# Performance work log

Measured on AMD Instinct MI355X. Metric: run time of the kernel, lower is better.

Reference implementation:

```python
import jax, jax.numpy as jnp
import numpy as np

# Static conv / spline hyperparameters (match init_kwargs)
KH = KW = 3
SH = SW = 1          # stride
DH = DW = 1          # dilation
GRID_SIZE = 5
SPLINE_ORDER = 3
N_CONVS = 8


def _extract_patches(x):
    """im2col unfold. x: (B,C,H,W) -> (B,C,Ho,Wo,KH*KW), valid padding."""
    B, C, H, W = x.shape
    Ho = (H - (KH - 1) * DH - 1) // SH + 1
    Wo = (W - (KW - 1) * DW - 1) // SW + 1
    cols = []
    for i in range(KH):
        for j in range(KW):
            cols.append(x[:, :,
                          i * DH: i * DH + (Ho - 1) * SH + 1: SH,
                          j * DW: j * DW + (Wo - 1) * SW + 1: SW])
    return jnp.stack(cols, axis=-1), Ho, Wo


def _b_splines(xf, grid):
    """Cox-de Boor recursion. xf: (P,K), grid: (K, G+2*so+1) -> (P,K,G+so)."""
    x = xf[:, :, None]
    bases = ((x >= grid[:, :-1]) & (x < grid[:, 1:])).astype(xf.dtype)
    for k in range(1, SPLINE_ORDER + 1):
        bases = ((x - grid[:, :-(k + 1)]) / (grid[:, k:-1] - grid[:, :-(k + 1)])
                 * bases[:, :, :-1]
                 + (grid[:, k + 1:] - x) / (grid[:, k + 1:] - grid[:, 1:-k])
                 * bases[:, :, 1:])
    return bases


def setup_inputs() -> dict:
    key = jax.random.key(0)
    k0, k1, k2, k3 = jax.random.split(key, 4)
    B, C, H, W = 8, 32, 64, 64
    K = KH * KW                       # in_features of KANLinear = 9
    coeff = GRID_SIZE + SPLINE_ORDER  # spline coefficients per input = 8
    # activations inside grid_range [-1, 1]
    x = jax.random.uniform(k0, (B, C, H, W), jnp.float32, -1.0, 1.0)
    # grid buffer: arange(-so, gs+so+1)*h + grid_range[0], tiled per input feature
    h = (1.0 - (-1.0)) / GRID_SIZE
    g = jnp.arange(-SPLINE_ORDER, GRID_SIZE + SPLINE_ORDER + 1,
                   dtype=jnp.float32) * h - 1.0
    grid = jnp.tile(g[None, :], (K, 1))  # (K, 12)
    base_weight = jax.random.normal(k1, (N_CONVS, K), jnp.float32) / np.sqrt(K)
    spline_weight = jax.random.normal(k2, (N_CONVS, K, coeff), jnp.float32) * 0.1
    spline_scaler = jax.random.normal(k3, (N_CONVS, K), jnp.float32) / np.sqrt(K) + 1.0
    return {"x": x, "grid": grid, "base_weight": base_weight,
            "spline_weight": spline_weight, "spline_scaler": spline_scaler}


def reference(x, grid, base_weight, spline_weight, spline_scaler):
    B, C, H, W = x.shape
    patches, Ho, Wo = _extract_patches(x)          # (B,C,Ho,Wo,K)
    K = KH * KW
    xf = patches.reshape(-1, K)                    # (P, K), P = B*C*Ho*Wo
    # KANLinear: base path (SiLU + linear) + spline path (B-spline basis + linear)
    base_out = jnp.einsum('pk,vk->pv', jax.nn.silu(xf), base_weight)
    bases = _b_splines(xf, grid)                   # (P, K, coeff)
    scaled_sw = spline_weight * spline_scaler[:, :, None]
    spline_out = jnp.einsum('pkc,vkc->pv', bases, scaled_sw)
    out = (base_out + spline_out).reshape(B, C, Ho, Wo, N_CONVS)
    # channel-major then conv ordering: out[:, kern + channel*n_convs]
    return out.transpose(0, 1, 4, 2, 3).reshape(B, C * N_CONVS, Ho, Wo)
```

## Files before the change

### kernel.cpp

```cpp
#include <hip/hip_runtime.h>

typedef _Float16 f16;
typedef _Float16 f16x8 __attribute__((ext_vector_type(8)));
typedef float    f32x4 __attribute__((ext_vector_type(4)));

#define HO 62
#define WO 62

__global__ __launch_bounds__(512, 4) void kan_conv_mfma(
    const float* __restrict__ x,
    const float* __restrict__ grid,
    const float* __restrict__ bw,
    const float* __restrict__ sw,
    const float* __restrict__ sc,
    float* __restrict__ out)
{
    __shared__ __align__(16) f16 feat[19456];

    const int tid  = threadIdx.x;
    const int lane = tid & 63;
    const int w    = tid >> 6;

    const int bx    = blockIdx.x;
    const int plane = bx >> 2;
    const int chunk = bx & 3;
    const int r0    = (chunk < 3) ? chunk * 16 : 46;

    const int nn = lane & 15;
    const int kb = lane >> 4;
    f16x8 bfrag[3][2];
    #pragma unroll
    for (int ki = 0; ki < 3; ++ki) {
        #pragma unroll
        for (int kjp = 0; kjp < 2; ++kjp) {
            f16x8 bf;
            #pragma unroll
            for (int e = 0; e < 8; ++e) {
                const int k    = kb * 8 + e;
                const int kj   = kjp * 2 + (k >> 4);
                const int slot = k & 15;
                float wv = 0.0f;
                if (nn < 8 && kj < 3 && slot < 9) {
                    const int kk = ki * 3 + kj;
                    wv = (slot == 0) ? bw[nn * 9 + kk]
                                     : sw[(nn * 9 + kk) * 8 + (slot - 1)] * sc[nn * 9 + kk];
                }
                bf[e] = (f16)wv;
            }
            bfrag[ki][kjp] = bf;
        }
    }

    const float g0    = grid[0];
    const float inv_h = 1.0f / (grid[1] - grid[0]);
    const float* xp   = x + (size_t)plane * 4096;

    for (int idx = tid; idx < 18 * 64; idx += 512) {
        const int row = idx >> 6;
        const int col = idx & 63;
        const float xv = xp[(r0 + row) * 64 + col];

        const float s = xv / (1.0f + __expf(-xv));
        const float u = (xv - g0) * inv_h;
        int j = (int)floorf(u);
        j = (j < 3) ? 3 : ((j > 7) ? 7 : j);
        const float t   = u - (float)j;
        const float omt = 1.0f - t;
        const float t2  = t * t;
        const float t3  = t2 * t;
        const float c6  = 1.0f / 6.0f;
        float bv[4];
        bv[0] = omt * omt * omt * c6;
        bv[1] = (3.0f * t3 - 6.0f * t2 + 4.0f) * c6;
        bv[2] = (-3.0f * t3 + 3.0f * t2 + 3.0f * t + 1.0f) * c6;
        bv[3] = t3 * c6;

        const int base0 = row * 1024 + col * 8;
        f16x8 z0 = {(f16)s, (f16)0.f, (f16)0.f, (f16)0.f,
                    (f16)0.f, (f16)0.f, (f16)0.f, (f16)0.f};
        f16x8 z1 = {(f16)0.f, (f16)0.f, (f16)0.f, (f16)0.f,
                    (f16)0.f, (f16)0.f, (f16)0.f, (f16)0.f};
        *(f16x8*)&feat[base0]       = z0;
        *(f16x8*)&feat[base0 + 512] = z1;
        #pragma unroll
        for (int m = 0; m < 4; ++m) {
            const int slot = j - 2 + m;
            feat[row * 1024 + (slot >> 3) * 512 + col * 8 + (slot & 7)] = (f16)bv[m];
        }
    }
    for (int idx = tid; idx < 128; idx += 512) {
        f16x8 z = {(f16)0.f, (f16)0.f, (f16)0.f, (f16)0.f,
                   (f16)0.f, (f16)0.f, (f16)0.f, (f16)0.f};
        *(f16x8*)&feat[18432 + idx * 8] = z;
    }
    __syncthreads();

    const int mI    = lane & 15;
    const int khalf = kb & 1;
    const int cAdd  = kb >> 1;

    for (int u = w; u < 64; u += 8) {
        const int ro = u >> 2;
        const int c0 = (u & 3) * 16;
        f32x4 acc = {0.f, 0.f, 0.f, 0.f};
        #pragma unroll
        for (int ki = 0; ki < 3; ++ki) {
            #pragma unroll
            for (int kjp = 0; kjp < 2; ++kjp) {
                const int col = c0 + mI + kjp * 2 + cAdd;
                const f16x8 a = *(const f16x8*)&feat[(ro + ki) * 1024 + khalf * 512 + col * 8];
                acc = __builtin_amdgcn_mfma_f32_16x16x32_f16(a, bfrag[ki][kjp], acc, 0, 0, 0);
            }
        }
        if (nn < 8) {
            const int rowg = r0 + ro;
            const int colb = c0 + kb * 4;
            float* po = out + ((size_t)(plane * 8 + nn) * (HO * WO)) + rowg * WO + colb;
            if (c0 < 48) {
                float2 lo = {acc[0], acc[1]};
                float2 hi = {acc[2], acc[3]};
                *(float2*)po       = lo;
                *(float2*)(po + 2) = hi;
            } else {
                #pragma unroll
                for (int i = 0; i < 4; ++i)
                    if (colb + i < WO) po[i] = acc[i];
            }
        }
    }
}

extern "C" void kernel_launch(void* const* d_in, const int* in_sizes, int n_in,
                              void* d_out, int out_size, void* d_ws, size_t ws_size,
                              hipStream_t stream) {
    const float* x    = (const float*)d_in[0];
    const float* grid = (const float*)d_in[1];
    const float* bw   = (const float*)d_in[2];
    const float* sw   = (const float*)d_in[3];
    const float* sc   = (const float*)d_in[4];
    float* out = (float*)d_out;

    kan_conv_mfma<<<1024, 512, 0, stream>>>(x, grid, bw, sw, sc, out);
}
```

Measured before the change: 94.18 us.

## Split planes into 8-row tiles and reuse A fragments across rows in registers

```diff
diff --git a/kernel.cpp b/kernel.cpp
--- a/kernel.cpp
+++ b/kernel.cpp
@@ -7,7 +7,7 @@
 #define HO 62
 #define WO 62
 
-__global__ __launch_bounds__(512, 4) void kan_conv_mfma(
+__global__ __launch_bounds__(256, 4) void kan_conv_mfma2(
     const float* __restrict__ x,
     const float* __restrict__ grid,
     const float* __restrict__ bw,
@@ -15,16 +15,16 @@
     const float* __restrict__ sc,
     float* __restrict__ out)
 {
-    __shared__ __align__(16) f16 feat[19456];
+    __shared__ __align__(16) f16 feat[10368];
 
     const int tid  = threadIdx.x;
     const int lane = tid & 63;
     const int w    = tid >> 6;
 
     const int bx    = blockIdx.x;
-    const int plane = bx >> 2;
-    const int chunk = bx & 3;
-    const int r0    = (chunk < 3) ? chunk * 16 : 46;
+    const int plane = bx >> 3;
+    const int chunk = bx & 7;
+    const int r0    = chunk * 8;
 
     const int nn = lane & 15;
     const int kb = lane >> 4;
@@ -55,10 +55,11 @@
     const float inv_h = 1.0f / (grid[1] - grid[0]);
     const float* xp   = x + (size_t)plane * 4096;
 
-    for (int idx = tid; idx < 18 * 64; idx += 512) {
+    for (int idx = tid; idx < 640; idx += 256) {
         const int row = idx >> 6;
         const int col = idx & 63;
-        const float xv = xp[(r0 + row) * 64 + col];
+        int gy = r0 + row; gy = (gy < 64) ? gy : 63;
+        const float xv = xp[gy * 64 + col];
 
         const float s = xv / (1.0f + __expf(-xv));
         const float u = (xv - g0) * inv_h;
@@ -88,43 +89,54 @@
             feat[row * 1024 + (slot >> 3) * 512 + col * 8 + (slot & 7)] = (f16)bv[m];
         }
     }
-    for (int idx = tid; idx < 128; idx += 512) {
+    if (tid < 16) {
         f16x8 z = {(f16)0.f, (f16)0.f, (f16)0.f, (f16)0.f,
                    (f16)0.f, (f16)0.f, (f16)0.f, (f16)0.f};
-        *(f16x8*)&feat[18432 + idx * 8] = z;
+        *(f16x8*)&feat[10240 + tid * 8] = z;
     }
     __syncthreads();
 
     const int mI    = lane & 15;
     const int khalf = kb & 1;
     const int cAdd  = kb >> 1;
+    const int c0    = w * 16;
+    const int aBase = khalf * 512 + (c0 + mI + cAdd) * 8;
 
-    for (int u = w; u < 64; u += 8) {
-        const int ro = u >> 2;
-        const int c0 = (u & 3) * 16;
+    f16x8 af[3][2];
+    #pragma unroll
+    for (int kjp = 0; kjp < 2; ++kjp) {
+        af[0][kjp] = *(const f16x8*)&feat[aBase + kjp * 16 + 0 * 1024];
+        af[1][kjp] = *(const f16x8*)&feat[aBase + kjp * 16 + 1 * 1024];
+    }
+
+    #pragma unroll
+    for (int i = 0; i < 8; ++i) {
+        #pragma unroll
+        for (int kjp = 0; kjp < 2; ++kjp)
+            af[(i + 2) % 3][kjp] = *(const f16x8*)&feat[aBase + kjp * 16 + (i + 2) * 1024];
+
         f32x4 acc = {0.f, 0.f, 0.f, 0.f};
         #pragma unroll
         for (int ki = 0; ki < 3; ++ki) {
             #pragma unroll
-            for (int kjp = 0; kjp < 2; ++kjp) {
-                const int col = c0 + mI + kjp * 2 + cAdd;
-                const f16x8 a = *(const f16x8*)&feat[(ro + ki) * 1024 + khalf * 512 + col * 8];
-                acc = __builtin_amdgcn_mfma_f32_16x16x32_f16(a, bfrag[ki][kjp], acc, 0, 0, 0);
-            }
+            for (int kjp = 0; kjp < 2; ++kjp)
+                acc = __builtin_amdgcn_mfma_f32_16x16x32_f16(
+                          af[(i + ki) % 3][kjp], bfrag[ki][kjp], acc, 0, 0, 0);
         }
-        if (nn < 8) {
-            const int rowg = r0 + ro;
-            const int colb = c0 + kb * 4;
-            float* po = out + ((size_t)(plane * 8 + nn) * (HO * WO)) + rowg * WO + colb;
-            if (c0 < 48) {
+
+        const int ho = r0 + i;
+        if (nn < 8 && ho < HO) {
+            const int cb = c0 + kb * 4;
+            float* po = out + ((size_t)(plane * 8 + nn) * (HO * WO)) + ho * WO + cb;
+            if (cb + 3 < WO) {
                 float2 lo = {acc[0], acc[1]};
                 float2 hi = {acc[2], acc[3]};
                 *(float2*)po       = lo;
                 *(float2*)(po + 2) = hi;
             } else {
                 #pragma unroll
-                for (int i = 0; i < 4; ++i)
-                    if (colb + i < WO) po[i] = acc[i];
+                for (int q = 0; q < 4; ++q)
+                    if (cb + q < WO) po[q] = acc[q];
             }
         }
     }
@@ -140,5 +152,5 @@
     const float* sc   = (const float*)d_in[4];
     float* out = (float*)d_out;
 
-    kan_conv_mfma<<<1024, 512, 0, stream>>>(x, grid, bw, sw, sc, out);
+    kan_conv_mfma2<<<2048, 256, 0, stream>>>(x, grid, bw, sw, sc, out);
 }
```

Result: slower. 97.16 us (+3.2%).
